# Performance work log

Hardware: AMD Instinct MI355X
Metric: run time of the kernel (lower is better)

Reference implementation:

```python
import jax, jax.numpy as jnp
import numpy as np

BOUND = 1.0
MIN_NEAR = 0.05
NUM_STEPS = 64
UP_STEPS = 64
DENSITY_SCALE = 1.0
N_RAYS = 16384
HIDDEN = 64


def setup_inputs() -> dict:
    key = jax.random.key(0)
    ks = jax.random.split(key, 8)
    # cameras hover near z=2 looking roughly toward -z so rays hit the [-1,1]^3 AABB
    rays_o = jax.random.normal(ks[0], (N_RAYS, 3), jnp.float32) * 0.1 + jnp.array([0.0, 0.0, 2.0])
    rays_d = jax.random.normal(ks[1], (N_RAYS, 3), jnp.float32) * 0.2 + jnp.array([0.0, 0.0, -1.0])
    rays_d = rays_d / jnp.linalg.norm(rays_d, axis=-1, keepdims=True)
    W1 = jax.random.normal(ks[2], (3, HIDDEN), jnp.float32) / jnp.sqrt(3.0)
    b1 = jnp.zeros((HIDDEN,), jnp.float32)
    w_sigma = jax.random.normal(ks[3], (HIDDEN, 1), jnp.float32) / jnp.sqrt(float(HIDDEN))
    b_sigma = jnp.zeros((1,), jnp.float32)
    W_rgb = jax.random.normal(ks[4], (HIDDEN, 3), jnp.float32) / jnp.sqrt(float(HIDDEN))
    b_rgb = jnp.zeros((3,), jnp.float32)
    return {"rays_o": rays_o, "rays_d": rays_d, "W1": W1, "b1": b1,
            "w_sigma": w_sigma, "b_sigma": b_sigma, "W_rgb": W_rgb, "b_rgb": b_rgb}


def near_far_cube(rays_o, rays_d, bound, min_near):
    tmin = (-bound - rays_o) / (rays_d + 1e-15)
    tmax = (bound - rays_o) / (rays_d + 1e-15)
    near = jnp.max(jnp.minimum(tmin, tmax), axis=-1, keepdims=True)
    far = jnp.min(jnp.maximum(tmin, tmax), axis=-1, keepdims=True)
    miss = far < near
    near = jnp.where(miss, 1e9, near)
    far = jnp.where(miss, 1e9, far)
    near = jnp.maximum(near, min_near)
    return near, far


def sample_pdf(bins, weights, n_samples):
    # bins: [N, M+1], weights: [N, M]; deterministic (det=True) inverse-CDF sampling
    weights = weights + 1e-5
    pdf = weights / jnp.sum(weights, -1, keepdims=True)
    cdf = jnp.cumsum(pdf, -1)
    cdf = jnp.concatenate([jnp.zeros_like(cdf[..., :1]), cdf], -1)  # [N, M+1]
    u = jnp.linspace(0.5 / n_samples, 1.0 - 0.5 / n_samples, n_samples, dtype=cdf.dtype)
    u = jnp.broadcast_to(u, cdf.shape[:-1] + (n_samples,))
    inds = jax.vmap(lambda c, uu: jnp.searchsorted(c, uu, side='right'))(cdf, u)
    below = jnp.maximum(inds - 1, 0)
    above = jnp.minimum(inds, cdf.shape[-1] - 1)
    cdf_b = jnp.take_along_axis(cdf, below, -1)
    cdf_a = jnp.take_along_axis(cdf, above, -1)
    bins_b = jnp.take_along_axis(bins, below, -1)
    bins_a = jnp.take_along_axis(bins, above, -1)
    denom = cdf_a - cdf_b
    denom = jnp.where(denom < 1e-5, jnp.ones_like(denom), denom)
    t = (u - cdf_b) / denom
    return bins_b + t * (bins_a - bins_b)


def mlp(pts, W1, b1, w_sigma, b_sigma, W_rgb, b_rgb):
    h = jax.nn.relu(pts @ W1 + b1)                      # [N, T, HIDDEN]
    sigma = jax.nn.softplus(h @ w_sigma + b_sigma)[..., 0]  # [N, T]
    rgb = jax.nn.sigmoid(h @ W_rgb + b_rgb)             # [N, T, 3]
    return sigma, rgb


def alpha_composite_weights(z_vals, sigma, sample_dist):
    deltas = z_vals[..., 1:] - z_vals[..., :-1]
    deltas = jnp.concatenate([deltas, jnp.broadcast_to(sample_dist, deltas[..., :1].shape)], -1)
    alphas = 1.0 - jnp.exp(-deltas * DENSITY_SCALE * sigma)
    trans = jnp.cumprod(jnp.concatenate([jnp.ones_like(alphas[..., :1]), 1.0 - alphas + 1e-15], -1)[..., :-1], -1)
    return alphas * trans


def reference(rays_o, rays_d, W1, b1, w_sigma, b_sigma, W_rgb, b_rgb):
    rays_d = rays_d / jnp.linalg.norm(rays_d, axis=-1, keepdims=True)
    near, far = near_far_cube(rays_o, rays_d, BOUND, MIN_NEAR)  # [N,1]
    sample_dist = (far - near) / NUM_STEPS                      # [N,1]

    # coarse stratified (deterministic) samples
    z = jnp.linspace(0.0, 1.0, NUM_STEPS, dtype=rays_o.dtype)
    z_vals = near + (far - near) * z                            # [N,T]
    xyzs = rays_o[:, None, :] + rays_d[:, None, :] * z_vals[..., None]
    xyzs = jnp.clip(xyzs, -BOUND, BOUND)
    sigma, _ = mlp(xyzs, W1, b1, w_sigma, b_sigma, W_rgb, b_rgb)
    weights = alpha_composite_weights(z_vals, sigma, sample_dist)

    # inverse-CDF importance resampling (no-grad in original)
    z_mid = 0.5 * (z_vals[..., :-1] + z_vals[..., 1:])          # [N,T-1]
    new_z = sample_pdf(z_mid, weights[:, 1:-1], UP_STEPS)       # [N,UP]
    new_z = jax.lax.stop_gradient(new_z)

    z_all = jnp.sort(jnp.concatenate([z_vals, new_z], -1), -1)  # [N,T+UP]
    xyzs_all = rays_o[:, None, :] + rays_d[:, None, :] * z_all[..., None]
    xyzs_all = jnp.clip(xyzs_all, -BOUND, BOUND)
    sigma_all, rgb_all = mlp(xyzs_all, W1, b1, w_sigma, b_sigma, W_rgb, b_rgb)
    weights_all = alpha_composite_weights(z_all, sigma_all, sample_dist)

    weights_sum = jnp.sum(weights_all, -1)                      # [N]
    image = jnp.sum(weights_all[..., None] * rgb_all, axis=-2)  # [N,3]
    image = image + (1.0 - weights_sum)[..., None]              # white background
    return image
```

## Files before the change

kernel.cpp:

```cpp
#include <hip/hip_runtime.h>
#include <math.h>

#define WAVES_PER_BLOCK 4

typedef float v2f __attribute__((ext_vector_type(2)));

__device__ __forceinline__ v2f v2_fma(v2f a, v2f b, v2f c) {
    return __builtin_elementwise_fma(a, b, c);
}
__device__ __forceinline__ v2f v2_max0(v2f a) {
    return __builtin_elementwise_max(a, (v2f){0.0f, 0.0f});
}
__device__ __forceinline__ v2f v2_splat(float x) { return (v2f){x, x}; }

__device__ __forceinline__ float fast_rcp(float x) { return __builtin_amdgcn_rcpf(x); }

__device__ __forceinline__ float wave_scan_mul(float v, int lane) {
#pragma unroll
    for (int off = 1; off < 64; off <<= 1) {
        float o = __shfl_up(v, off, 64);
        if (lane >= off) v *= o;
    }
    return v;
}

__device__ __forceinline__ float wave_scan_add(float v, int lane) {
#pragma unroll
    for (int off = 1; off < 64; off <<= 1) {
        float o = __shfl_up(v, off, 64);
        if (lane >= off) v += o;
    }
    return v;
}

__device__ __forceinline__ float wave_sum(float v) {
#pragma unroll
    for (int off = 32; off; off >>= 1) v += __shfl_xor(v, off, 64);
    return v;
}

__device__ __forceinline__ float softplus_f(float x) {
    return fmaxf(x, 0.0f) + __logf(1.0f + __expf(-fabsf(x)));
}

__device__ __forceinline__ float sigmoid_f(float x) {
    return fast_rcp(1.0f + __expf(-x));
}

__device__ __forceinline__ int count_lt64(const float* a, float x) {
    int lo = 0, hi = 64;
    while (lo < hi) { int mid = (lo + hi) >> 1; if (a[mid] < x) lo = mid + 1; else hi = mid; }
    return lo;
}
__device__ __forceinline__ int count_le64(const float* a, float x) {
    int lo = 0, hi = 64;
    while (lo < hi) { int mid = (lo + hi) >> 1; if (a[mid] <= x) lo = mid + 1; else hi = mid; }
    return lo;
}

__global__ __launch_bounds__(WAVES_PER_BLOCK * 64)
void nerf_render_kernel(const float* __restrict__ rays_o,
                        const float* __restrict__ rays_d,
                        const float* __restrict__ W1,
                        const float* __restrict__ b1,
                        const float* __restrict__ w_sigma,
                        const float* __restrict__ b_sigma,
                        const float* __restrict__ W_rgb,
                        const float* __restrict__ b_rgb,
                        float* __restrict__ out)
{
    const int tid  = threadIdx.x;
    const int lane = tid & 63;
    const int wv   = tid >> 6;
    const int ray  = blockIdx.x * WAVES_PER_BLOCK + wv;

    __shared__ float s_zmid[WAVES_PER_BLOCK][64];
    __shared__ float s_cdf [WAVES_PER_BLOCK][64];
    __shared__ float s_zall[WAVES_PER_BLOCK][128];

    float ox = rays_o[ray * 3 + 0], oy = rays_o[ray * 3 + 1], oz = rays_o[ray * 3 + 2];
    float dx = rays_d[ray * 3 + 0], dy = rays_d[ray * 3 + 1], dz = rays_d[ray * 3 + 2];
    {
        float inv = __builtin_amdgcn_rsqf(dx * dx + dy * dy + dz * dz);
        dx *= inv; dy *= inv; dz *= inv;
    }

    float rx = fast_rcp(dx + 1e-15f);
    float ry = fast_rcp(dy + 1e-15f);
    float rz = fast_rcp(dz + 1e-15f);
    float t0x = (-1.0f - ox) * rx, t1x = (1.0f - ox) * rx;
    float t0y = (-1.0f - oy) * ry, t1y = (1.0f - oy) * ry;
    float t0z = (-1.0f - oz) * rz, t1z = (1.0f - oz) * rz;
    float nearv = fmaxf(fmaxf(fminf(t0x, t1x), fminf(t0y, t1y)), fminf(t0z, t1z));
    float farv  = fminf(fminf(fmaxf(t0x, t1x), fmaxf(t0y, t1y)), fmaxf(t0z, t1z));
    if (farv < nearv) { nearv = 1e9f; farv = 1e9f; }
    nearv = fmaxf(nearv, 0.05f);
    const float sample_dist = (farv - nearv) * (1.0f / 64.0f);

    const float bs0 = b_sigma[0];
    const float br0 = b_rgb[0], br1 = b_rgb[1], br2 = b_rgb[2];

    const float lstep = 1.0f / 63.0f;
    float z = nearv + (farv - nearv) * ((float)lane * lstep);

    float px = fminf(fmaxf(fmaf(dx, z, ox), -1.0f), 1.0f);
    float py = fminf(fmaxf(fmaf(dy, z, oy), -1.0f), 1.0f);
    float pz = fminf(fmaxf(fmaf(dz, z, oz), -1.0f), 1.0f);

    const v2f* W1x2 = (const v2f*)(W1);
    const v2f* W1y2 = (const v2f*)(W1 + 64);
    const v2f* W1z2 = (const v2f*)(W1 + 128);
    const v2f* b12  = (const v2f*)(b1);
    const v2f* ws2  = (const v2f*)(w_sigma);

    v2f px2 = v2_splat(px), py2 = v2_splat(py), pz2 = v2_splat(pz);
    v2f sacc2 = (v2f){bs0, 0.0f};
#pragma unroll 8
    for (int j = 0; j < 32; ++j) {
        v2f h = v2_fma(px2, W1x2[j], v2_fma(py2, W1y2[j], v2_fma(pz2, W1z2[j], b12[j])));
        h = v2_max0(h);
        sacc2 = v2_fma(h, ws2[j], sacc2);
    }
    float sigma = softplus_f(sacc2.x + sacc2.y);

    float z_next = __shfl_down(z, 1, 64);
    float delta  = (lane < 63) ? (z_next - z) : sample_dist;
    float alpha  = 1.0f - __expf(-delta * sigma);
    float v      = 1.0f - alpha + 1e-15f;
    float incl   = wave_scan_mul(v, lane);
    float trans  = __shfl_up(incl, 1, 64);
    if (lane == 0) trans = 1.0f;
    float w = alpha * trans;

    float wgt = (lane >= 1 && lane <= 62) ? (w + 1e-5f) : 0.0f;
    float total = wave_sum(wgt);
    float pdf = wgt * fast_rcp(total);
    float cdf_incl = wave_scan_add(pdf, lane);

    float zmid = 0.5f * (z + z_next);
    s_zmid[wv][lane] = (lane < 63) ? zmid : 0.0f;
    s_cdf [wv][lane] = (lane < 63) ? cdf_incl : 2.0f;
    __syncthreads();

    float u = 0.0078125f + (float)lane * 0.015625f;
    int ind = count_le64(s_cdf[wv], u);
    int below = ind - 1;
    int above = (ind < 62) ? ind : 62;
    float cb = s_cdf[wv][below], ca = s_cdf[wv][above];
    float bb = s_zmid[wv][below], ba = s_zmid[wv][above];
    float denom = ca - cb;
    if (denom < 1e-5f) denom = 1.0f;
    float t = (u - cb) * fast_rcp(denom);
    float nz = fmaf(t, ba - bb, bb);

    __syncthreads();

    s_zmid[wv][lane] = z;
    s_cdf [wv][lane] = nz;
    __syncthreads();
    int pa = lane + count_lt64(s_cdf [wv], z);
    int pb = lane + count_le64(s_zmid[wv], nz);
    s_zall[wv][pa] = z;
    s_zall[wv][pb] = nz;
    __syncthreads();

    float za0 = s_zall[wv][2 * lane + 0];
    float za1 = s_zall[wv][2 * lane + 1];

    v2f pxx = { fminf(fmaxf(fmaf(dx, za0, ox), -1.0f), 1.0f),
                fminf(fmaxf(fmaf(dx, za1, ox), -1.0f), 1.0f) };
    v2f pyy = { fminf(fmaxf(fmaf(dy, za0, oy), -1.0f), 1.0f),
                fminf(fmaxf(fmaf(dy, za1, oy), -1.0f), 1.0f) };
    v2f pzz = { fminf(fmaxf(fmaf(dz, za0, oz), -1.0f), 1.0f),
                fminf(fmaxf(fmaf(dz, za1, oz), -1.0f), 1.0f) };

    v2f s2 = v2_splat(bs0);
    v2f r2 = v2_splat(br0), g2 = v2_splat(br1), bch2 = v2_splat(br2);
#pragma unroll 8
    for (int j = 0; j < 64; ++j) {
        float w1x = W1[j], w1y = W1[64 + j], w1z = W1[128 + j], bj = b1[j];
        float ws  = w_sigma[j];
        float wr  = W_rgb[3 * j + 0], wg = W_rgb[3 * j + 1], wb = W_rgb[3 * j + 2];
        v2f h = v2_fma(pxx, v2_splat(w1x),
                v2_fma(pyy, v2_splat(w1y),
                v2_fma(pzz, v2_splat(w1z), v2_splat(bj))));
        h = v2_max0(h);
        s2   = v2_fma(h, v2_splat(ws), s2);
        r2   = v2_fma(h, v2_splat(wr), r2);
        g2   = v2_fma(h, v2_splat(wg), g2);
        bch2 = v2_fma(h, v2_splat(wb), bch2);
    }
    float sg0 = softplus_f(s2.x), sg1 = softplus_f(s2.y);
    float r0 = sigmoid_f(r2.x),   r1 = sigmoid_f(r2.y);
    float g0 = sigmoid_f(g2.x),   g1 = sigmoid_f(g2.y);
    float bl0 = sigmoid_f(bch2.x), bl1 = sigmoid_f(bch2.y);

    float zn0 = __shfl_down(za0, 1, 64);
    float d0 = za1 - za0;
    float d1 = (lane < 63) ? (zn0 - za1) : sample_dist;
    float a0 = 1.0f - __expf(-d0 * sg0);
    float a1 = 1.0f - __expf(-d1 * sg1);
    float v0 = 1.0f - a0 + 1e-15f;
    float v1 = 1.0f - a1 + 1e-15f;
    float local = v0 * v1;
    float incl2 = wave_scan_mul(local, lane);
    float eprod = __shfl_up(incl2, 1, 64);
    if (lane == 0) eprod = 1.0f;
    float tr0 = eprod;
    float tr1 = eprod * v0;
    float w0 = a0 * tr0;
    float w1 = a1 * tr1;

    float wsum = wave_sum(w0 + w1);
    float rs = wave_sum(fmaf(w0, r0,  w1 * r1));
    float gs = wave_sum(fmaf(w0, g0,  w1 * g1));
    float bs = wave_sum(fmaf(w0, bl0, w1 * bl1));

    if (lane == 0) {
        float bg = 1.0f - wsum;
        out[ray * 3 + 0] = rs + bg;
        out[ray * 3 + 1] = gs + bg;
        out[ray * 3 + 2] = bs + bg;
    }
}

extern "C" void kernel_launch(void* const* d_in, const int* in_sizes, int n_in,
                              void* d_out, int out_size, void* d_ws, size_t ws_size,
                              hipStream_t stream) {
    const float* rays_o  = (const float*)d_in[0];
    const float* rays_d  = (const float*)d_in[1];
    const float* W1      = (const float*)d_in[2];
    const float* b1      = (const float*)d_in[3];
    const float* w_sigma = (const float*)d_in[4];
    const float* b_sigma = (const float*)d_in[5];
    const float* W_rgb   = (const float*)d_in[6];
    const float* b_rgb   = (const float*)d_in[7];
    float* out = (float*)d_out;

    const int n_rays = in_sizes[0] / 3;
    dim3 grid((n_rays + WAVES_PER_BLOCK - 1) / WAVES_PER_BLOCK);
    dim3 block(WAVES_PER_BLOCK * 64);
    hipLaunchKernelGGL(nerf_render_kernel, grid, block, 0, stream,
                       rays_o, rays_d, W1, b1, w_sigma, b_sigma, W_rgb, b_rgb, out);
}
```

Before: 104.6 us.

## Precompute per-ray affine hidden pre-activations so each MLP layer needs one FMA

Each ray's first-layer pre-activation is affine in z. The kernel now computes c_j = W1·o + b1 and m_j = W1·d once per ray, storing 64 of each per wave in shared memory. Both MLP passes then evaluate h = max(m*z + c, 0) instead of three FMAs plus position clamps per hidden unit. Missed rays get the clamped far-point constant with zero slope. The four final wave reductions are also packed into two paired-float reductions. The risk is dropping the xyz clamp for hit rays, which relies on samples between near and far lying inside the box up to rounding, and adding shared-memory reads inside the hot loop.

```diff
diff --git a/kernel.cpp b/kernel.cpp
--- a/kernel.cpp
+++ b/kernel.cpp
@@ -39,12 +39,25 @@
     return v;
 }
 
+__device__ __forceinline__ v2f wave_sum2(v2f v) {
+#pragma unroll
+    for (int off = 32; off; off >>= 1) {
+        v2f o = { __shfl_xor(v.x, off, 64), __shfl_xor(v.y, off, 64) };
+        v += o;
+    }
+    return v;
+}
+
 __device__ __forceinline__ float softplus_f(float x) {
     return fmaxf(x, 0.0f) + __logf(1.0f + __expf(-fabsf(x)));
 }
 
 __device__ __forceinline__ float sigmoid_f(float x) {
     return fast_rcp(1.0f + __expf(-x));
+}
+
+__device__ __forceinline__ float clamp1(float x) {
+    return fminf(fmaxf(x, -1.0f), 1.0f);
 }
 
 __device__ __forceinline__ int count_lt64(const float* a, float x) {
@@ -74,6 +87,7 @@
     const int wv   = tid >> 6;
     const int ray  = blockIdx.x * WAVES_PER_BLOCK + wv;
 
+    __shared__ float s_cm  [WAVES_PER_BLOCK][128];
     __shared__ float s_zmid[WAVES_PER_BLOCK][64];
     __shared__ float s_cdf [WAVES_PER_BLOCK][64];
     __shared__ float s_zall[WAVES_PER_BLOCK][128];
@@ -93,35 +107,42 @@
     float t0z = (-1.0f - oz) * rz, t1z = (1.0f - oz) * rz;
     float nearv = fmaxf(fmaxf(fminf(t0x, t1x), fminf(t0y, t1y)), fminf(t0z, t1z));
     float farv  = fminf(fminf(fmaxf(t0x, t1x), fmaxf(t0y, t1y)), fmaxf(t0z, t1z));
-    if (farv < nearv) { nearv = 1e9f; farv = 1e9f; }
+    const bool miss = (farv < nearv);
+    if (miss) { nearv = 1e9f; farv = 1e9f; }
     nearv = fmaxf(nearv, 0.05f);
     const float sample_dist = (farv - nearv) * (1.0f / 64.0f);
 
     const float bs0 = b_sigma[0];
     const float br0 = b_rgb[0], br1 = b_rgb[1], br2 = b_rgb[2];
 
-    const float lstep = 1.0f / 63.0f;
-    float z = nearv + (farv - nearv) * ((float)lane * lstep);
-
-    float px = fminf(fmaxf(fmaf(dx, z, ox), -1.0f), 1.0f);
-    float py = fminf(fmaxf(fmaf(dy, z, oy), -1.0f), 1.0f);
-    float pz = fminf(fmaxf(fmaf(dz, z, oz), -1.0f), 1.0f);
-
-    const v2f* W1x2 = (const v2f*)(W1);
-    const v2f* W1y2 = (const v2f*)(W1 + 64);
-    const v2f* W1z2 = (const v2f*)(W1 + 128);
-    const v2f* b12  = (const v2f*)(b1);
-    const v2f* ws2  = (const v2f*)(w_sigma);
-
-    v2f px2 = v2_splat(px), py2 = v2_splat(py), pz2 = v2_splat(pz);
-    v2f sacc2 = (v2f){bs0, 0.0f};
+    {
+        float w1x = W1[lane], w1y = W1[64 + lane], w1z = W1[128 + lane];
+        float eox = ox, eoy = oy, eoz = oz, msc = 1.0f;
+        if (miss) {
+            eox = clamp1(fmaf(dx, 1e9f, ox));
+            eoy = clamp1(fmaf(dy, 1e9f, oy));
+            eoz = clamp1(fmaf(dz, 1e9f, oz));
+            msc = 0.0f;
+        }
+        float cj = fmaf(eox, w1x, fmaf(eoy, w1y, fmaf(eoz, w1z, b1[lane])));
+        float mj = msc * fmaf(dx, w1x, fmaf(dy, w1y, dz * w1z));
+        s_cm[wv][lane]      = cj;
+        s_cm[wv][64 + lane] = mj;
+    }
+
+    float z = nearv + (farv - nearv) * ((float)lane * (1.0f / 63.0f));
+
+    const v2f* c2p = (const v2f*)&s_cm[wv][0];
+    const v2f* m2p = (const v2f*)&s_cm[wv][64];
+    const v2f* ws2 = (const v2f*)w_sigma;
+    v2f z2 = v2_splat(z);
+    v2f acc = (v2f){bs0, 0.0f};
 #pragma unroll 8
-    for (int j = 0; j < 32; ++j) {
-        v2f h = v2_fma(px2, W1x2[j], v2_fma(py2, W1y2[j], v2_fma(pz2, W1z2[j], b12[j])));
-        h = v2_max0(h);
-        sacc2 = v2_fma(h, ws2[j], sacc2);
-    }
-    float sigma = softplus_f(sacc2.x + sacc2.y);
+    for (int jj = 0; jj < 32; ++jj) {
+        v2f h = v2_max0(v2_fma(m2p[jj], z2, c2p[jj]));
+        acc = v2_fma(h, ws2[jj], acc);
+    }
+    float sigma = softplus_f(acc.x + acc.y);
 
     float z_next = __shfl_down(z, 1, 64);
     float delta  = (lane < 63) ? (z_next - z) : sample_dist;
@@ -167,28 +188,18 @@
     float za0 = s_zall[wv][2 * lane + 0];
     float za1 = s_zall[wv][2 * lane + 1];
 
-    v2f pxx = { fminf(fmaxf(fmaf(dx, za0, ox), -1.0f), 1.0f),
-                fminf(fmaxf(fmaf(dx, za1, ox), -1.0f), 1.0f) };
-    v2f pyy = { fminf(fmaxf(fmaf(dy, za0, oy), -1.0f), 1.0f),
-                fminf(fmaxf(fmaf(dy, za1, oy), -1.0f), 1.0f) };
-    v2f pzz = { fminf(fmaxf(fmaf(dz, za0, oz), -1.0f), 1.0f),
-                fminf(fmaxf(fmaf(dz, za1, oz), -1.0f), 1.0f) };
-
+    v2f zz = (v2f){za0, za1};
     v2f s2 = v2_splat(bs0);
     v2f r2 = v2_splat(br0), g2 = v2_splat(br1), bch2 = v2_splat(br2);
 #pragma unroll 8
     for (int j = 0; j < 64; ++j) {
-        float w1x = W1[j], w1y = W1[64 + j], w1z = W1[128 + j], bj = b1[j];
-        float ws  = w_sigma[j];
-        float wr  = W_rgb[3 * j + 0], wg = W_rgb[3 * j + 1], wb = W_rgb[3 * j + 2];
-        v2f h = v2_fma(pxx, v2_splat(w1x),
-                v2_fma(pyy, v2_splat(w1y),
-                v2_fma(pzz, v2_splat(w1z), v2_splat(bj))));
-        h = v2_max0(h);
-        s2   = v2_fma(h, v2_splat(ws), s2);
-        r2   = v2_fma(h, v2_splat(wr), r2);
-        g2   = v2_fma(h, v2_splat(wg), g2);
-        bch2 = v2_fma(h, v2_splat(wb), bch2);
+        float cj = s_cm[wv][j];
+        float mj = s_cm[wv][64 + j];
+        v2f h = v2_max0(v2_fma(v2_splat(mj), zz, v2_splat(cj)));
+        s2   = v2_fma(h, v2_splat(w_sigma[j]),    s2);
+        r2   = v2_fma(h, v2_splat(W_rgb[3 * j + 0]), r2);
+        g2   = v2_fma(h, v2_splat(W_rgb[3 * j + 1]), g2);
+        bch2 = v2_fma(h, v2_splat(W_rgb[3 * j + 2]), bch2);
     }
     float sg0 = softplus_f(s2.x), sg1 = softplus_f(s2.y);
     float r0 = sigmoid_f(r2.x),   r1 = sigmoid_f(r2.y);
@@ -206,21 +217,19 @@
     float incl2 = wave_scan_mul(local, lane);
     float eprod = __shfl_up(incl2, 1, 64);
     if (lane == 0) eprod = 1.0f;
-    float tr0 = eprod;
-    float tr1 = eprod * v0;
-    float w0 = a0 * tr0;
-    float w1 = a1 * tr1;
-
-    float wsum = wave_sum(w0 + w1);
-    float rs = wave_sum(fmaf(w0, r0,  w1 * r1));
-    float gs = wave_sum(fmaf(w0, g0,  w1 * g1));
-    float bs = wave_sum(fmaf(w0, bl0, w1 * bl1));
+    float w0 = a0 * eprod;
+    float w1 = a1 * (eprod * v0);
+
+    v2f wr_ = { w0 + w1,               fmaf(w0, r0,  w1 * r1) };
+    v2f gb_ = { fmaf(w0, g0, w1 * g1), fmaf(w0, bl0, w1 * bl1) };
+    wr_ = wave_sum2(wr_);
+    gb_ = wave_sum2(gb_);
 
     if (lane == 0) {
-        float bg = 1.0f - wsum;
-        out[ray * 3 + 0] = rs + bg;
-        out[ray * 3 + 1] = gs + bg;
-        out[ray * 3 + 2] = bs + bg;
+        float bg = 1.0f - wr_.x;
+        out[ray * 3 + 0] = wr_.y + bg;
+        out[ray * 3 + 1] = gb_.x + bg;
+        out[ray * 3 + 2] = gb_.y + bg;
     }
 }
 
```

Result: faster. 96.97 us (-7.3%).
